# Kernel optimization log

Hardware: AMD Instinct MI355X
Metric: run time of the kernel (lower is better)

Reference implementation:

```python
import jax, jax.numpy as jnp
import numpy as np

B, S, D = 4, 4096, 1024
H = 8                    # num_heads
DK = D // H              # head_k_dim = 128
DV = D // H              # head_v_dim = 128
KLEPE = 5                # lepe kernel size
ROPE_BASE = 10000.0


def rotate_half(x):
    x1, x2 = jnp.split(x, 2, axis=-1)
    return jnp.concatenate([-x2, x1], axis=-1)


def rope_sin_cos(seq_len, dim):
    inv_freq = 1.0 / (ROPE_BASE ** (jnp.arange(0, dim, 2, dtype=jnp.float32) / dim))
    freqs = jnp.arange(seq_len, dtype=jnp.float32)[:, None] * inv_freq[None, :]
    emb = jnp.concatenate([freqs, freqs], axis=-1)  # [S, dim]
    return jnp.sin(emb), jnp.cos(emb)


def mala_attn(q, k, v):
    """Magnitude-aware linear attention with inline RoPE.

    Attention weights A_ij = (scale*q_i.k_j + 1) / (scale*q_i.(sum_j k_j) + S):
    rows sum to 1 but, unlike plain linear attention, the sharpness of the
    distribution still depends on ||q_i|| (magnitude rectification). Computed
    in O(S*d^2) linear form without materializing the SxS matrix.
    q, k: [B,S,H,DK]; v: [B,S,H,DV].
    """
    sin, cos = rope_sin_cos(q.shape[1], q.shape[-1])
    sin, cos = sin[None, :, None, :], cos[None, :, None, :]
    q = q * cos + rotate_half(q) * sin
    k = k * cos + rotate_half(k) * sin
    scale = q.shape[-1] ** -0.5
    seq_len = q.shape[1]
    kv = jnp.einsum('bshd,bshe->bhde', k, v)      # [B,H,DK,DV]
    ksum = k.sum(axis=1)                          # [B,H,DK]
    vsum = v.sum(axis=1)                          # [B,H,DV]
    num = jnp.einsum('bshd,bhde->bshe', q, kv) * scale + vsum[:, None, :, :]
    den = jnp.einsum('bshd,bhd->bsh', q, ksum) * scale + seq_len
    return num / den[..., None]


def lepe_conv(v, w, b):
    # depthwise Conv1d over the sequence axis; channel id = h*DV + d
    Bb, Ss = v.shape[0], v.shape[1]
    x = v.transpose(0, 2, 3, 1).reshape(Bb, H * DV, Ss)   # [B, C, S]
    y = jax.lax.conv_general_dilated(
        x, w, window_strides=(1,), padding=[(KLEPE // 2, KLEPE // 2)],
        dimension_numbers=('NCH', 'OIH', 'NCH'), feature_group_count=H * DV)
    y = y + b[None, :, None]
    return y.reshape(Bb, H, DV, Ss).transpose(0, 3, 1, 2)  # [B,S,H,DV]


def setup_inputs() -> dict:
    key = jax.random.key(0)
    ks = jax.random.split(key, 8)
    w = 0.02
    return {
        'hidden_states': jax.random.normal(ks[0], (B, S, D), dtype=jnp.float32),
        'Wq': jax.random.normal(ks[1], (D, D), dtype=jnp.float32) * w,
        'Wk': jax.random.normal(ks[2], (D, D), dtype=jnp.float32) * w,
        'Wv': jax.random.normal(ks[3], (D, D), dtype=jnp.float32) * w,
        'Wg': jax.random.normal(ks[4], (D, D), dtype=jnp.float32) * w,
        'Wo': jax.random.normal(ks[5], (D, D), dtype=jnp.float32) * w,
        'lepe_w': jax.random.normal(ks[6], (D, 1, KLEPE), dtype=jnp.float32) * 0.1,
        'lepe_b': jnp.zeros((D,), dtype=jnp.float32),
    }


def reference(hidden_states, Wq, Wk, Wv, Wg, Wo, lepe_w, lepe_b):
    Bb, Ss, _ = hidden_states.shape
    q = (hidden_states @ Wq.T).reshape(Bb, Ss, H, DK)
    k = (hidden_states @ Wk.T).reshape(Bb, Ss, H, DK)
    v = (hidden_states @ Wv.T).reshape(Bb, Ss, H, DV)
    o_gate = hidden_states @ Wg.T                          # [B,S,D]
    o = mala_attn(q, k, v) + lepe_conv(v, lepe_w, lepe_b)  # [B,S,H,DV]
    o = o.reshape(Bb, Ss, H * DV) * o_gate
    return o @ Wo.T
```

## Files before the change

### kernel.cpp

```cpp
#include <hip/hip_runtime.h>
#include <math.h>
#include <stdint.h>


typedef __bf16 bf16;
typedef __bf16 bf16x2 __attribute__((ext_vector_type(2)));
typedef __bf16 bf16x4 __attribute__((ext_vector_type(4)));
typedef __bf16 bf16x8 __attribute__((ext_vector_type(8)));
typedef float f32x4 __attribute__((ext_vector_type(4)));

static constexpr float kScale = 0.08838834764831845f;

__device__ __forceinline__ void async_copy16(const void* g, void* l) {
  __builtin_amdgcn_global_load_lds(
      (const __attribute__((address_space(1))) void*)(uintptr_t)g,
      (__attribute__((address_space(3))) void*)(uintptr_t)l, 16, 0, 0);
}

__global__ __launch_bounds__(512, 1) void gemm_qkvg(
    const bf16* __restrict__ A, const bf16* __restrict__ Bw,
    bf16* __restrict__ C, const float2* __restrict__ tab)
{
  __shared__ __align__(16) char smem[131072];

  const int t = threadIdx.x;
  const int bid = blockIdx.x;
  const int swz = (bid & 7) * 128 + (bid >> 3);
  const int bx = swz & 63;
  const int by = swz >> 6;
  const long m0 = (long)bx * 256;
  const long n0 = (long)by * 256;

  const int d0 = t * 16;
  const int dd = d0 ^ (((d0 >> 9) & 1) << 5);
  const int rT = dd >> 7;
  const int cT = (dd & 127) >> 1;
  const bf16* aSt = A  + (m0 + rT) * 1024 + cT;
  const bf16* bSt = Bw + (n0 + rT) * 1024 + cT;
  char* ldsDst = smem + d0;

  const int lane = t & 63, wid = t >> 6;
  const int wm = wid >> 2, wn = wid & 3;
  const int fm = lane & 15, fq = lane >> 4;
  const int xsw = (fm & 4) << 3;
  const char* ldsA = smem + wm * 16384 + fm * 128 + (fq * 16 ^ xsw);
  const char* ldsB = smem + 32768 + (wn >> 1) * 16384 +
                     ((wn & 1) * 64 + fm) * 128 + (fq * 16 ^ xsw);

  f32x4 acc[8][4] = {};
  bf16x8 a4[4][2], b2[2][2];

#define STAGE_A(kt, h) do {                                                  \
    const bf16* s_ = aSt + (long)(h) * 131072 + (kt) * 64;                   \
    char* d_ = ldsDst + ((kt) & 1) * 65536 + (h) * 16384;                    \
    async_copy16(s_, d_);                                                    \
    async_copy16(s_ + 65536, d_ + 8192);                                     \
  } while (0)
#define STAGE_B(kt, h) do {                                                  \
    const bf16* s_ = bSt + (long)(h) * 131072 + (kt) * 64;                   \
    char* d_ = ldsDst + ((kt) & 1) * 65536 + 32768 + (h) * 16384;            \
    async_copy16(s_, d_);                                                    \
    async_copy16(s_ + 65536, d_ + 8192);                                     \
  } while (0)
#define LOAD_A(buf, qi) do {                                                 \
    const char* p_ = ldsA + (buf) * 65536 + (qi) * 8192;                     \
    a4[0][0] = *(const bf16x8*)(p_);                                         \
    a4[0][1] = *(const bf16x8*)(p_ + 64);                                    \
    a4[1][0] = *(const bf16x8*)(p_ + 2048);                                  \
    a4[1][1] = *(const bf16x8*)(p_ + 2048 + 64);                             \
    a4[2][0] = *(const bf16x8*)(p_ + 4096);                                  \
    a4[2][1] = *(const bf16x8*)(p_ + 4096 + 64);                             \
    a4[3][0] = *(const bf16x8*)(p_ + 6144);                                  \
    a4[3][1] = *(const bf16x8*)(p_ + 6144 + 64);                             \
  } while (0)
#define LOAD_B(buf, qj) do {                                                 \
    const char* p_ = ldsB + (buf) * 65536 + (qj) * 4096;                     \
    b2[0][0] = *(const bf16x8*)(p_);                                         \
    b2[0][1] = *(const bf16x8*)(p_ + 64);                                    \
    b2[1][0] = *(const bf16x8*)(p_ + 2048);                                  \
    b2[1][1] = *(const bf16x8*)(p_ + 2048 + 64);                             \
  } while (0)
#define MM1(i, j, ks)                                                        \
    acc[i][j] = __builtin_amdgcn_mfma_f32_16x16x32_bf16(                     \
        a4[(i) & 3][ks], b2[(j) & 1][ks], acc[i][j], 0, 0, 0)
#define MFMA_Q(qi, qj) do {                                                  \
    MM1(4*(qi)+0, 2*(qj)+0, 0); MM1(4*(qi)+1, 2*(qj)+0, 0);                  \
    MM1(4*(qi)+2, 2*(qj)+0, 0); MM1(4*(qi)+3, 2*(qj)+0, 0);                  \
    MM1(4*(qi)+0, 2*(qj)+1, 0); MM1(4*(qi)+1, 2*(qj)+1, 0);                  \
    MM1(4*(qi)+2, 2*(qj)+1, 0); MM1(4*(qi)+3, 2*(qj)+1, 0);                  \
    MM1(4*(qi)+0, 2*(qj)+0, 1); MM1(4*(qi)+1, 2*(qj)+0, 1);                  \
    MM1(4*(qi)+2, 2*(qj)+0, 1); MM1(4*(qi)+3, 2*(qj)+0, 1);                  \
    MM1(4*(qi)+0, 2*(qj)+1, 1); MM1(4*(qi)+1, 2*(qj)+1, 1);                  \
    MM1(4*(qi)+2, 2*(qj)+1, 1); MM1(4*(qi)+3, 2*(qj)+1, 1);                  \
  } while (0)
#define BAR()    __builtin_amdgcn_s_barrier()
#define SCHEDB() __builtin_amdgcn_sched_barrier(0)
#define PRIO(p)  __builtin_amdgcn_s_setprio(p)

  STAGE_A(0, 0); STAGE_A(0, 1); STAGE_B(0, 0); STAGE_B(0, 1);
  STAGE_A(1, 0);
  asm volatile("s_waitcnt vmcnt(2)" ::: "memory");
  BAR(); SCHEDB();

#pragma unroll 1
  for (int it = 0; it < 7; ++it) {
    const int k1 = 2 * it + 1;
    const int k2 = 2 * it + 2;
    const int k3 = 2 * it + 3;
    LOAD_A(0, 0); LOAD_B(0, 0);
    STAGE_A(k1, 1);
    BAR(); SCHEDB(); PRIO(1); MFMA_Q(0, 0); PRIO(0); BAR(); SCHEDB();
    LOAD_B(0, 1);
    STAGE_B(k1, 0);
    BAR(); SCHEDB(); PRIO(1); MFMA_Q(0, 1); PRIO(0); BAR(); SCHEDB();
    LOAD_A(0, 1);
    STAGE_B(k1, 1);
    BAR(); SCHEDB(); PRIO(1); MFMA_Q(1, 1); PRIO(0); BAR(); SCHEDB();
    LOAD_B(0, 0);
    STAGE_A(k2, 0);
    BAR(); SCHEDB(); PRIO(1); MFMA_Q(1, 0); PRIO(0);
    asm volatile("s_waitcnt vmcnt(2)" ::: "memory");
    BAR(); SCHEDB();
    LOAD_A(1, 0); LOAD_B(1, 0);
    STAGE_A(k2, 1);
    BAR(); SCHEDB(); PRIO(1); MFMA_Q(0, 0); PRIO(0); BAR(); SCHEDB();
    LOAD_B(1, 1);
    STAGE_B(k2, 0);
    BAR(); SCHEDB(); PRIO(1); MFMA_Q(0, 1); PRIO(0); BAR(); SCHEDB();
    LOAD_A(1, 1);
    STAGE_B(k2, 1);
    BAR(); SCHEDB(); PRIO(1); MFMA_Q(1, 1); PRIO(0); BAR(); SCHEDB();
    LOAD_B(1, 0);
    STAGE_A(k3, 0);
    BAR(); SCHEDB(); PRIO(1); MFMA_Q(1, 0); PRIO(0);
    asm volatile("s_waitcnt vmcnt(2)" ::: "memory");
    BAR(); SCHEDB();
  }

  {
    LOAD_A(0, 0); LOAD_B(0, 0);
    STAGE_A(15, 1);
    BAR(); SCHEDB(); PRIO(1); MFMA_Q(0, 0); PRIO(0); BAR(); SCHEDB();
    LOAD_B(0, 1);
    STAGE_B(15, 0);
    BAR(); SCHEDB(); PRIO(1); MFMA_Q(0, 1); PRIO(0); BAR(); SCHEDB();
    LOAD_A(0, 1);
    STAGE_B(15, 1);
    BAR(); SCHEDB(); PRIO(1); MFMA_Q(1, 1); PRIO(0); BAR(); SCHEDB();
    LOAD_B(0, 0);
    BAR(); SCHEDB(); PRIO(1); MFMA_Q(1, 0); PRIO(0);
    asm volatile("s_waitcnt vmcnt(0)" ::: "memory");
    BAR(); SCHEDB();
    LOAD_A(1, 0); LOAD_B(1, 0);
    BAR(); SCHEDB(); PRIO(1); MFMA_Q(0, 0); PRIO(0); BAR(); SCHEDB();
    LOAD_B(1, 1);
    BAR(); SCHEDB(); PRIO(1); MFMA_Q(0, 1); PRIO(0); BAR(); SCHEDB();
    LOAD_A(1, 1);
    BAR(); SCHEDB(); PRIO(1); MFMA_Q(1, 1); PRIO(0); BAR(); SCHEDB();
    LOAD_B(1, 0);
    BAR(); SCHEDB(); PRIO(1); MFMA_Q(1, 0); PRIO(0); BAR(); SCHEDB();
  }

#undef STAGE_A
#undef STAGE_B
#undef LOAD_A
#undef LOAD_B
#undef MM1
#undef MFMA_Q
#undef BAR
#undef SCHEDB
#undef PRIO

  bf16* T = (bf16*)smem;
  __syncthreads();
#pragma unroll 1
  for (int hw = 0; hw < 2; ++hw) {
    if (wm == hw) {
#pragma unroll
      for (int rf = 0; rf < 8; ++rf)
#pragma unroll
        for (int cf = 0; cf < 4; ++cf)
#pragma unroll
          for (int r = 0; r < 4; ++r)
            T[(rf * 16 + fq * 4 + r) * 264 + wn * 64 + cf * 16 + fm] =
                (bf16)acc[rf][cf][r];
    }
    __syncthreads();
    if (by < 8) {
#pragma unroll
      for (int ii = 0; ii < 32; ++ii) {
        const int pi = t + ii * 512;
        const int row = pi >> 7, pr = pi & 127;
        const int hd = pr >> 6, i = pr & 63;
        const int c0 = hd * 128 + i;
        const int s = (int)((m0 + hw * 128 + row) & 4095);
        const float2 sc = tab[s * 64 + i];
        float x1 = (float)T[row * 264 + c0];
        float x2 = (float)T[row * 264 + c0 + 64];
        T[row * 264 + c0]      = (bf16)(x1 * sc.y - x2 * sc.x);
        T[row * 264 + c0 + 64] = (bf16)(x2 * sc.y + x1 * sc.x);
      }
      __syncthreads();
    }
#pragma unroll
    for (int ii = 0; ii < 8; ++ii) {
      const int cid = t + ii * 512;
      const int row = cid >> 5, ch = cid & 31;
      *(bf16x8*)(C + (m0 + hw * 128 + row) * 4096 + n0 + ch * 8) =
          *(const bf16x8*)(T + row * 264 + ch * 8);
    }
    __syncthreads();
  }
}

__global__ __launch_bounds__(256, 2) void gemm_final(
    const bf16* __restrict__ A, const bf16* __restrict__ Bw,
    float* __restrict__ C)
{
  __shared__ __align__(16) bf16 As[128 * 32];
  __shared__ __align__(16) bf16 Bs[128 * 32];
  const int t = threadIdx.x;
  const int bid = blockIdx.x;
  const int xcd = bid & 7, n = bid >> 3;
  const int bx = xcd * 16 + (n & 15);
  const int by = n >> 4;
  const long m0 = (long)bx * 128;
  A  += m0 * 1024;
  Bw += (long)by * 131072;
  C  += m0 * 1024 + (long)by * 128;

  const int i0 = t, i1 = t + 256;
  const bf16* gA0 = A  + (long)(i0 >> 2) * 1024 + (i0 & 3) * 8;
  const bf16* gA1 = A  + (long)(i1 >> 2) * 1024 + (i1 & 3) * 8;
  const bf16* gB0 = Bw + (long)(i0 >> 2) * 1024 + (i0 & 3) * 8;
  const bf16* gB1 = Bw + (long)(i1 >> 2) * 1024 + (i1 & 3) * 8;
  bf16* lA0 = As + i0 * 8; bf16* lA1 = As + i1 * 8;
  bf16* lB0 = Bs + i0 * 8; bf16* lB1 = Bs + i1 * 8;

  const int lane = t & 63, wv = t >> 6;
  const int moff = (wv & 1) * 64, noff = (wv >> 1) * 64;
  const int fm = lane & 15, fq = lane >> 4;

  f32x4 acc[4][4] = {};

  for (int k0 = 0; k0 < 1024; k0 += 32) {
    async_copy16(gA0, lA0); async_copy16(gA1, lA1);
    async_copy16(gB0, lB0); async_copy16(gB1, lB1);
    gA0 += 32; gA1 += 32; gB0 += 32; gB1 += 32;
    __syncthreads();
    bf16x8 af[4], bfv[4];
#pragma unroll
    for (int i = 0; i < 4; ++i) {
      af[i]  = *(const bf16x8*)(As + (moff + i * 16 + fm) * 32 + fq * 8);
      bfv[i] = *(const bf16x8*)(Bs + (noff + i * 16 + fm) * 32 + fq * 8);
    }
#pragma unroll
    for (int i = 0; i < 4; ++i)
#pragma unroll
      for (int j = 0; j < 4; ++j)
        acc[i][j] = __builtin_amdgcn_mfma_f32_16x16x32_bf16(af[i], bfv[j], acc[i][j], 0, 0, 0);
    __syncthreads();
  }

#pragma unroll
  for (int i = 0; i < 4; ++i)
#pragma unroll
    for (int j = 0; j < 4; ++j)
#pragma unroll
      for (int r = 0; r < 4; ++r)
        C[(long)(moff + i * 16 + fq * 4 + r) * 1024 + noff + j * 16 + fm] = acc[i][j][r];
}

__global__ __launch_bounds__(256, 2) void gemm_num(
    const bf16* __restrict__ QKVG, const bf16* __restrict__ kvTall,
    const float* __restrict__ ksum, const float* __restrict__ vsum,
    const float* __restrict__ lepe_w, const float* __restrict__ lepe_b,
    bf16* __restrict__ obuf)
{
  __shared__ __align__(16) char smem[17408];
  bf16* As = (bf16*)smem;
  bf16* Bs = (bf16*)(smem + 8192);
  bf16* T  = (bf16*)smem;
  __shared__ float sden[128], svsum[128], slb[128], sksum[128];
  __shared__ float slw[5][128];

  const int t = threadIdx.x;
  const int h = blockIdx.y, b = blockIdx.z;
  const int bh = b * 8 + h;
  const long m0 = (long)blockIdx.x * 128;
  const bf16* A  = QKVG + (long)b * 16777216 + m0 * 4096 + h * 128;
  const bf16* Bw = kvTall + (long)bh * 16384;

  if (t < 128) {
    sksum[t] = ksum[bh * 128 + t];
    svsum[t] = vsum[bh * 128 + t];
    slb[t]   = lepe_b[h * 128 + t];
#pragma unroll
    for (int j = 0; j < 5; ++j) slw[j][t] = lepe_w[(h * 128 + t) * 5 + j];
  }

  const int i0 = t, i1 = t + 256;
  const bf16* gA0 = A + (long)(i0 >> 2) * 4096 + (i0 & 3) * 8;
  const bf16* gA1 = A + (long)(i1 >> 2) * 4096 + (i1 & 3) * 8;
  const bf16* gB0 = Bw + (long)(i0 >> 2) * 128 + (i0 & 3) * 8;
  const bf16* gB1 = Bw + (long)(i1 >> 2) * 128 + (i1 & 3) * 8;
  bf16* lA0 = As + i0 * 8; bf16* lA1 = As + i1 * 8;
  bf16* lB0 = Bs + i0 * 8; bf16* lB1 = Bs + i1 * 8;

  const int lane = t & 63, wv = t >> 6;
  const int moff = (wv & 1) * 64, noff = (wv >> 1) * 64;
  const int fm = lane & 15, fq = lane >> 4;

  f32x4 acc[4][4] = {};
  float dacc = 0.f;

  for (int k0 = 0; k0 < 128; k0 += 32) {
    async_copy16(gA0, lA0); async_copy16(gA1, lA1);
    async_copy16(gB0, lB0); async_copy16(gB1, lB1);
    gA0 += 32; gA1 += 32; gB0 += 32; gB1 += 32;
    __syncthreads();
    bf16x8 af[4], bfv[4];
#pragma unroll
    for (int i = 0; i < 4; ++i) {
      af[i]  = *(const bf16x8*)(As + (moff + i * 16 + fm) * 32 + fq * 8);
      bfv[i] = *(const bf16x8*)(Bs + (noff + i * 16 + fm) * 32 + fq * 8);
    }
#pragma unroll
    for (int i = 0; i < 4; ++i)
#pragma unroll
      for (int j = 0; j < 4; ++j)
        acc[i][j] = __builtin_amdgcn_mfma_f32_16x16x32_bf16(af[i], bfv[j], acc[i][j], 0, 0, 0);
    if (t < 128) {
#pragma unroll
      for (int c8 = 0; c8 < 4; ++c8) {
        bf16x8 q8 = *(const bf16x8*)(As + t * 32 + c8 * 8);
#pragma unroll
        for (int e = 0; e < 8; ++e) dacc += (float)q8[e] * sksum[k0 + c8 * 8 + e];
      }
    }
    __syncthreads();
  }
  if (t < 128) sden[t] = dacc * kScale + 4096.0f;

  const int c2 = lane * 2;
  const float w0[5] = {slw[0][c2], slw[1][c2], slw[2][c2], slw[3][c2], slw[4][c2]};
  const float w1[5] = {slw[0][c2+1], slw[1][c2+1], slw[2][c2+1], slw[3][c2+1], slw[4][c2+1]};
  const float lb0 = slb[c2], lb1 = slb[c2 + 1];

#pragma unroll
  for (int half = 0; half < 2; ++half) {
    if ((wv & 1) == half) {
#pragma unroll
      for (int i = 0; i < 4; ++i)
#pragma unroll
        for (int j = 0; j < 4; ++j)
#pragma unroll
          for (int r = 0; r < 4; ++r) {
            const int col = noff + j * 16 + fm;
            T[(i * 16 + fq * 4 + r) * 136 + col] = (bf16)(acc[i][j][r] * kScale + svsum[col]);
          }
    }
    __syncthreads();
    for (int rr = 0; rr < 16; ++rr) {
      const int lrow = wv * 16 + rr;
      const int row = half * 64 + lrow;
      const int s = (int)(m0 + row);
      const long grow = (long)b * 4096 + s;
      const float rden = 1.0f / sden[row];
      const bf16* vrow = QKVG + grow * 4096 + 2048 + h * 128 + c2;
      bf16x2 a2 = *(const bf16x2*)(T + lrow * 136 + c2);
      float lep0 = lb0, lep1 = lb1;
#pragma unroll
      for (int jt = 0; jt < 5; ++jt) {
        const int srow = s + jt - 2;
        if (srow >= 0 && srow < 4096) {
          bf16x2 v2 = *(const bf16x2*)(vrow + (long)(jt - 2) * 4096);
          lep0 += (float)v2[0] * w0[jt];
          lep1 += (float)v2[1] * w1[jt];
        }
      }
      bf16x2 g2 = *(const bf16x2*)(QKVG + grow * 4096 + 3072 + h * 128 + c2);
      bf16x2 o2;
      o2[0] = (bf16)(((float)a2[0] * rden + lep0) * (float)g2[0]);
      o2[1] = (bf16)(((float)a2[1] * rden + lep1) * (float)g2[1]);
      *(bf16x2*)(obuf + grow * 1024 + h * 128 + c2) = o2;
    }
    __syncthreads();
  }
}

__global__ void prep_kernel(const float* __restrict__ X, const float* __restrict__ Wq,
                            const float* __restrict__ Wk, const float* __restrict__ Wv,
                            const float* __restrict__ Wg, const float* __restrict__ Wo,
                            bf16* __restrict__ Xb, bf16* __restrict__ Wcat,
                            bf16* __restrict__ Wob, float2* __restrict__ tab)
{
  const int blk = blockIdx.x;
  if (blk < 16384) {
    long g = ((long)blk * 256 + threadIdx.x) * 4;
    float4 v = *(const float4*)(X + g);
    bf16x4 o = {(bf16)v.x, (bf16)v.y, (bf16)v.z, (bf16)v.w};
    *(bf16x4*)(Xb + g) = o;
  } else if (blk < 21504) {
    long g = ((long)(blk - 16384) * 256 + threadIdx.x) * 4;
    if (g < 4194304) {
      long idx = g & 1048575;
      int sel = (int)(g >> 20);
      const float* s = sel == 0 ? Wq : sel == 1 ? Wk : sel == 2 ? Wv : Wg;
      float4 v = *(const float4*)(s + idx);
      bf16x4 o = {(bf16)v.x, (bf16)v.y, (bf16)v.z, (bf16)v.w};
      *(bf16x4*)(Wcat + g) = o;
    } else {
      long idx = g - 4194304;
      float4 v = *(const float4*)(Wo + idx);
      bf16x4 o = {(bf16)v.x, (bf16)v.y, (bf16)v.z, (bf16)v.w};
      *(bf16x4*)(Wob + idx) = o;
    }
  } else {
    int idx = (blk - 21504) * 256 + threadIdx.x;
    int s = idx >> 6, i = idx & 63;
    float inv = powf(10000.0f, -((float)(2 * i)) / 128.0f);
    float ang = (float)s * inv;
    float sn, cs;
    sincosf(ang, &sn, &cs);
    tab[idx] = make_float2(sn, cs);
  }
}

__global__ __launch_bounds__(256, 2) void kv_mfma(
    const bf16* __restrict__ QKVG, float* __restrict__ kvp,
    float* __restrict__ ksump, float* __restrict__ vsump)
{
  __shared__ __align__(16) bf16 VT[128 * 40];
  __shared__ __align__(16) bf16 KT[128 * 40];
  const int t = threadIdx.x;
  const int chunk = blockIdx.x, bh = blockIdx.y;
  const int b = bh >> 3, h = bh & 7;
  const long rowbase = ((long)b * 4096 + chunk * 256) * 4096 + h * 128;
  const bf16* Kg = QKVG + rowbase + 1024;
  const bf16* Vg = QKVG + rowbase + 2048;

  const int sp = t >> 4, fc = t & 15;
  const int lane = t & 63, wv = t >> 6;
  const int eoff = (wv & 1) * 64, doff = (wv >> 1) * 64;
  const int fm = lane & 15, fq = lane >> 4;
  const int srow = t & 127;
  const bool sumK = t >= 128;

  f32x4 acc[4][4] = {};
  float rsum = 0.f;

  for (int sb = 0; sb < 256; sb += 32) {
    const long go = (long)(sb + 2 * sp) * 4096 + fc * 8;
    bf16x8 v0 = *(const bf16x8*)(Vg + go);
    bf16x8 v1 = *(const bf16x8*)(Vg + go + 4096);
    bf16x8 k0 = *(const bf16x8*)(Kg + go);
    bf16x8 k1 = *(const bf16x8*)(Kg + go + 4096);
#pragma unroll
    for (int j = 0; j < 8; ++j) {
      const int f = fc * 8 + j;
      bf16x2 vp2 = {v0[j], v1[j]};
      bf16x2 kp2 = {k0[j], k1[j]};
      *(bf16x2*)(VT + f * 40 + 2 * sp) = vp2;
      *(bf16x2*)(KT + f * 40 + 2 * sp) = kp2;
    }
    __syncthreads();
    bf16x8 af[4], bfv[4];
#pragma unroll
    for (int i = 0; i < 4; ++i) {
      af[i]  = *(const bf16x8*)(VT + (eoff + i * 16 + fm) * 40 + fq * 8);
      bfv[i] = *(const bf16x8*)(KT + (doff + i * 16 + fm) * 40 + fq * 8);
    }
#pragma unroll
    for (int i = 0; i < 4; ++i)
#pragma unroll
      for (int j = 0; j < 4; ++j)
        acc[i][j] = __builtin_amdgcn_mfma_f32_16x16x32_bf16(af[i], bfv[j], acc[i][j], 0, 0, 0);
    const bf16* rp = (sumK ? KT : VT) + srow * 40;
#pragma unroll
    for (int i = 0; i < 4; ++i) {
      bf16x8 r8 = *(const bf16x8*)(rp + i * 8);
#pragma unroll
      for (int j = 0; j < 8; ++j) rsum += (float)r8[j];
    }
    __syncthreads();
  }

  float* plane = kvp + ((long)chunk * 32 + bh) * 16384;
#pragma unroll
  for (int i = 0; i < 4; ++i)
#pragma unroll
    for (int j = 0; j < 4; ++j)
#pragma unroll
      for (int r = 0; r < 4; ++r)
        plane[(long)(eoff + i * 16 + fq * 4 + r) * 128 + (doff + j * 16 + fm)] = acc[i][j][r];
  float* sdst = (sumK ? ksump : vsump) + ((long)chunk * 32 + bh) * 128 + srow;
  *sdst = rsum;
}

__global__ void kv_reduce(const float* __restrict__ kvp, const float* __restrict__ ksump,
                          const float* __restrict__ vsump, bf16* __restrict__ kvT,
                          float* __restrict__ ksum, float* __restrict__ vsum)
{
  long g = (long)blockIdx.x * 256 + threadIdx.x;
  long bh = g >> 14, idx = g & 16383;
  float s = 0.f;
#pragma unroll
  for (int c = 0; c < 16; ++c) s += kvp[((long)c * 32 + bh) * 16384 + idx];
  kvT[g] = (bf16)s;
  if (g < 8192) {
    int bh2 = (int)(g >> 8), rem = (int)(g & 255), f = rem & 127;
    const float* src = (rem >> 7) ? ksump : vsump;
    float* dst = (rem >> 7) ? ksum : vsum;
    float s2 = 0.f;
#pragma unroll
    for (int c = 0; c < 16; ++c) s2 += src[((long)c * 32 + bh2) * 128 + f];
    dst[bh2 * 128 + f] = s2;
  }
}

extern "C" void kernel_launch(void* const* d_in, const int* in_sizes, int n_in,
                              void* d_out, int out_size, void* d_ws, size_t ws_size,
                              hipStream_t stream)
{
  const float* X      = (const float*)d_in[0];
  const float* Wq     = (const float*)d_in[1];
  const float* Wk     = (const float*)d_in[2];
  const float* Wv     = (const float*)d_in[3];
  const float* Wg     = (const float*)d_in[4];
  const float* Wo     = (const float*)d_in[5];
  const float* lepe_w = (const float*)d_in[6];
  const float* lepe_b = (const float*)d_in[7];
  float* out = (float*)d_out;

  char* ws = (char*)d_ws;
  bf16*   Xb    = (bf16*)(ws);
  float*  kvp   = (float*)(ws);
  bf16*   Wcat  = (bf16*)(ws + 33554432);
  bf16*   Wob   = (bf16*)(ws + 41943040);
  float2* tab   = (float2*)(ws + 44040192);
  float*  ksump = (float*)(ws + 44040192);
  float*  vsump = (float*)(ws + 44302336);
  bf16*   QKVG  = (bf16*)(ws + 46137344);
  float*  ksum  = (float*)(ws + 180355072);
  float*  vsum  = (float*)(ws + 180371456);
  bf16*   kvT   = (bf16*)(ws + 180387840);
  bf16*   obuf  = (bf16*)(ws + 181960704);

  prep_kernel<<<22528, 256, 0, stream>>>(X, Wq, Wk, Wv, Wg, Wo, Xb, Wcat, Wob, tab);

  gemm_qkvg<<<1024, 512, 0, stream>>>(Xb, Wcat, QKVG, tab);

  kv_mfma<<<dim3(16, 32), 256, 0, stream>>>(QKVG, kvp, ksump, vsump);
  kv_reduce<<<2048, 256, 0, stream>>>(kvp, ksump, vsump, kvT, ksum, vsum);

  gemm_num<<<dim3(32, 8, 4), 256, 0, stream>>>(QKVG, kvT, ksum, vsum, lepe_w, lepe_b, obuf);

  gemm_final<<<1024, 256, 0, stream>>>(obuf, Wob, out);
}
```

Measured before the change: 452.7 us.

## Use full XOR LDS swizzle, keep all B fragments resident, remap block tiles

The LDS swizzle changes from a single-bit XOR to a 3-bit XOR over 16-byte chunks, applied to both the async global-to-LDS stores and the fragment reads, to cut bank conflicts. B fragments are now held in four register slots instead of two, so the redundant reloads of B quarter 0 before the last MFMA quarter are removed. The block-to-tile mapping is also reordered to group tiles differently for L2 reuse. The change costs extra VGPRs for the B fragments and relies on the new mapping and swizzle staying consistent between writer and reader.

```diff
diff --git a/kernel.cpp b/kernel.cpp
--- a/kernel.cpp
+++ b/kernel.cpp
@@ -25,14 +25,14 @@
 
   const int t = threadIdx.x;
   const int bid = blockIdx.x;
-  const int swz = (bid & 7) * 128 + (bid >> 3);
-  const int bx = swz & 63;
-  const int by = swz >> 6;
+  const int n = bid >> 3;
+  const int bx = (bid & 7) * 8 + (n & 7);
+  const int by = n >> 3;
   const long m0 = (long)bx * 256;
   const long n0 = (long)by * 256;
 
   const int d0 = t * 16;
-  const int dd = d0 ^ (((d0 >> 9) & 1) << 5);
+  const int dd = d0 ^ (((d0 >> 7) & 7) << 4);
   const int rT = dd >> 7;
   const int cT = (dd & 127) >> 1;
   const bf16* aSt = A  + (m0 + rT) * 1024 + cT;
@@ -42,13 +42,17 @@
   const int lane = t & 63, wid = t >> 6;
   const int wm = wid >> 2, wn = wid & 3;
   const int fm = lane & 15, fq = lane >> 4;
-  const int xsw = (fm & 4) << 3;
-  const char* ldsA = smem + wm * 16384 + fm * 128 + (fq * 16 ^ xsw);
-  const char* ldsB = smem + 32768 + (wn >> 1) * 16384 +
-                     ((wn & 1) * 64 + fm) * 128 + (fq * 16 ^ xsw);
+  const int xsw = (fm & 7) << 4;
+  const int o0 = (fq * 16) ^ xsw;
+  const int o1 = o0 ^ 64;
+  const char* ldsA0 = smem + wm * 16384 + fm * 128 + o0;
+  const char* ldsA1 = smem + wm * 16384 + fm * 128 + o1;
+  const char* ldsB0 = smem + 32768 + (wn >> 1) * 16384 +
+                      ((wn & 1) * 64 + fm) * 128 + o0;
+  const char* ldsB1 = ldsB0 + (o1 - o0);
 
   f32x4 acc[8][4] = {};
-  bf16x8 a4[4][2], b2[2][2];
+  bf16x8 a4[4][2], b4[4][2];
 
 #define STAGE_A(kt, h) do {                                                  \
     const bf16* s_ = aSt + (long)(h) * 131072 + (kt) * 64;                   \
@@ -63,26 +67,28 @@
     async_copy16(s_ + 65536, d_ + 8192);                                     \
   } while (0)
 #define LOAD_A(buf, qi) do {                                                 \
-    const char* p_ = ldsA + (buf) * 65536 + (qi) * 8192;                     \
-    a4[0][0] = *(const bf16x8*)(p_);                                         \
-    a4[0][1] = *(const bf16x8*)(p_ + 64);                                    \
-    a4[1][0] = *(const bf16x8*)(p_ + 2048);                                  \
-    a4[1][1] = *(const bf16x8*)(p_ + 2048 + 64);                             \
-    a4[2][0] = *(const bf16x8*)(p_ + 4096);                                  \
-    a4[2][1] = *(const bf16x8*)(p_ + 4096 + 64);                             \
-    a4[3][0] = *(const bf16x8*)(p_ + 6144);                                  \
-    a4[3][1] = *(const bf16x8*)(p_ + 6144 + 64);                             \
+    const char* p0_ = ldsA0 + (buf) * 65536 + (qi) * 8192;                   \
+    const char* p1_ = ldsA1 + (buf) * 65536 + (qi) * 8192;                   \
+    a4[0][0] = *(const bf16x8*)(p0_);                                        \
+    a4[0][1] = *(const bf16x8*)(p1_);                                        \
+    a4[1][0] = *(const bf16x8*)(p0_ + 2048);                                 \
+    a4[1][1] = *(const bf16x8*)(p1_ + 2048);                                 \
+    a4[2][0] = *(const bf16x8*)(p0_ + 4096);                                 \
+    a4[2][1] = *(const bf16x8*)(p1_ + 4096);                                 \
+    a4[3][0] = *(const bf16x8*)(p0_ + 6144);                                 \
+    a4[3][1] = *(const bf16x8*)(p1_ + 6144);                                 \
   } while (0)
 #define LOAD_B(buf, qj) do {                                                 \
-    const char* p_ = ldsB + (buf) * 65536 + (qj) * 4096;                     \
-    b2[0][0] = *(const bf16x8*)(p_);                                         \
-    b2[0][1] = *(const bf16x8*)(p_ + 64);                                    \
-    b2[1][0] = *(const bf16x8*)(p_ + 2048);                                  \
-    b2[1][1] = *(const bf16x8*)(p_ + 2048 + 64);                             \
+    const char* p0_ = ldsB0 + (buf) * 65536 + (qj) * 4096;                   \
+    const char* p1_ = ldsB1 + (buf) * 65536 + (qj) * 4096;                   \
+    b4[2*(qj)+0][0] = *(const bf16x8*)(p0_);                                 \
+    b4[2*(qj)+0][1] = *(const bf16x8*)(p1_);                                 \
+    b4[2*(qj)+1][0] = *(const bf16x8*)(p0_ + 2048);                          \
+    b4[2*(qj)+1][1] = *(const bf16x8*)(p1_ + 2048);                          \
   } while (0)
 #define MM1(i, j, ks)                                                        \
     acc[i][j] = __builtin_amdgcn_mfma_f32_16x16x32_bf16(                     \
-        a4[(i) & 3][ks], b2[(j) & 1][ks], acc[i][j], 0, 0, 0)
+        a4[(i) & 3][ks], b4[j][ks], acc[i][j], 0, 0, 0)
 #define MFMA_Q(qi, qj) do {                                                  \
     MM1(4*(qi)+0, 2*(qj)+0, 0); MM1(4*(qi)+1, 2*(qj)+0, 0);                  \
     MM1(4*(qi)+2, 2*(qj)+0, 0); MM1(4*(qi)+3, 2*(qj)+0, 0);                  \
@@ -116,7 +122,6 @@
     LOAD_A(0, 1);
     STAGE_B(k1, 1);
     BAR(); SCHEDB(); PRIO(1); MFMA_Q(1, 1); PRIO(0); BAR(); SCHEDB();
-    LOAD_B(0, 0);
     STAGE_A(k2, 0);
     BAR(); SCHEDB(); PRIO(1); MFMA_Q(1, 0); PRIO(0);
     asm volatile("s_waitcnt vmcnt(2)" ::: "memory");
@@ -130,7 +135,6 @@
     LOAD_A(1, 1);
     STAGE_B(k2, 1);
     BAR(); SCHEDB(); PRIO(1); MFMA_Q(1, 1); PRIO(0); BAR(); SCHEDB();
-    LOAD_B(1, 0);
     STAGE_A(k3, 0);
     BAR(); SCHEDB(); PRIO(1); MFMA_Q(1, 0); PRIO(0);
     asm volatile("s_waitcnt vmcnt(2)" ::: "memory");
@@ -147,7 +151,6 @@
     LOAD_A(0, 1);
     STAGE_B(15, 1);
     BAR(); SCHEDB(); PRIO(1); MFMA_Q(1, 1); PRIO(0); BAR(); SCHEDB();
-    LOAD_B(0, 0);
     BAR(); SCHEDB(); PRIO(1); MFMA_Q(1, 0); PRIO(0);
     asm volatile("s_waitcnt vmcnt(0)" ::: "memory");
     BAR(); SCHEDB();
@@ -157,7 +160,6 @@
     BAR(); SCHEDB(); PRIO(1); MFMA_Q(0, 1); PRIO(0); BAR(); SCHEDB();
     LOAD_A(1, 1);
     BAR(); SCHEDB(); PRIO(1); MFMA_Q(1, 1); PRIO(0); BAR(); SCHEDB();
-    LOAD_B(1, 0);
     BAR(); SCHEDB(); PRIO(1); MFMA_Q(1, 0); PRIO(0); BAR(); SCHEDB();
   }
 
```

After: 427.4 us. -5.6%, faster.
